# Optimization experiments

Measured on AMD Instinct MI355X. Metric: run time of the kernel, lower is better.

## Reference

```python
import jax, jax.numpy as jnp
import numpy as np

V, E, H, L, B, S = 32000, 256, 512, 2, 128, 512


def _lstm_step(x, h, c, w_ih, w_hh, b_ih, b_hh):
    # PyTorch gate order: i, f, g, o
    gates = x @ w_ih.T + b_ih + h @ w_hh.T + b_hh
    i, f, g, o = jnp.split(gates, 4, axis=-1)
    c2 = jax.nn.sigmoid(f) * c + jax.nn.sigmoid(i) * jnp.tanh(g)
    h2 = jax.nn.sigmoid(o) * jnp.tanh(c2)
    return h2, c2


def setup_inputs() -> dict:
    key = jax.random.key(0)
    ks = jax.random.split(key, 16)
    s = 0.05
    d = {}
    d["dec_input"] = jax.random.randint(ks[0], (B,), 0, V)
    d["hidden"] = jax.random.normal(ks[1], (L, B, H), jnp.float32)
    d["cell"] = jax.random.normal(ks[2], (L, B, H), jnp.float32)
    d["encoder_outputs"] = jax.random.normal(ks[3], (S, B, H), jnp.float32)
    d["emb"] = jax.random.normal(ks[4], (V, E), jnp.float32) * s
    d["attn_w"] = jax.random.normal(ks[5], (1, 2 * H), jnp.float32) * s
    d["attn_b"] = jnp.zeros((1,), jnp.float32)
    d["w_ih0"] = jax.random.normal(ks[6], (4 * H, E + H), jnp.float32) * s
    d["w_hh0"] = jax.random.normal(ks[7], (4 * H, H), jnp.float32) * s
    d["b_ih0"] = jnp.zeros((4 * H,), jnp.float32)
    d["b_hh0"] = jnp.zeros((4 * H,), jnp.float32)
    d["w_ih1"] = jax.random.normal(ks[8], (4 * H, H), jnp.float32) * s
    d["w_hh1"] = jax.random.normal(ks[9], (4 * H, H), jnp.float32) * s
    d["b_ih1"] = jnp.zeros((4 * H,), jnp.float32)
    d["b_hh1"] = jnp.zeros((4 * H,), jnp.float32)
    d["fc_w"] = jax.random.normal(ks[10], (V, H), jnp.float32) * s
    d["fc_b"] = jnp.zeros((V,), jnp.float32)
    return d


def reference(dec_input, hidden, cell, encoder_outputs, emb, attn_w, attn_b,
              w_ih0, w_hh0, b_ih0, b_hh0, w_ih1, w_hh1, b_ih1, b_hh1,
              fc_w, fc_b):
    # embedded: [B, E]  (dropout p=0 -> identity)
    embedded = emb[dec_input]
    # Bahdanau-style additive scoring using FIRST-layer hidden (as in source)
    h0 = hidden[0]                                   # [B, H]
    w_enc, w_hid = attn_w[0, :H], attn_w[0, H:]      # split linear over concat
    # logits[b,s] = enc[s,b]@w_enc + h0[b]@w_hid + b
    logits = jnp.einsum('sbh,h->bs', encoder_outputs, w_enc) \
        + (h0 @ w_hid)[:, None] + attn_b[0]          # [B, S]
    alpha = jax.nn.softmax(logits, axis=1)           # softmax over src positions
    # context = sum_s alpha[b,s] * enc[s,b,:]  (avoids repeat_interleave blowup)
    context = jnp.einsum('bs,sbh->bh', alpha, encoder_outputs)  # [B, H]
    x = jnp.concatenate([context, embedded], axis=1)            # [B, H+E]
    # single-timestep 2-layer LSTM
    h_0, c_0 = _lstm_step(x, hidden[0], cell[0], w_ih0, w_hh0, b_ih0, b_hh0)
    h_1, c_1 = _lstm_step(h_0, hidden[1], cell[1], w_ih1, w_hh1, b_ih1, b_hh1)
    new_hidden = jnp.stack([h_0, h_1])
    new_cell = jnp.stack([c_0, c_1])
    prediction = h_1 @ fc_w.T + fc_b                 # [B, V]
    return prediction, new_hidden, new_cell
```

## Files before the change

### kernel.cpp

```cpp
#include <hip/hip_runtime.h>
#include <hip/hip_bf16.h>
#include <math.h>

constexpr int NV = 32000;
constexpr int NE = 256;
constexpr int NH = 512;
constexpr int NB = 128;
constexpr int NS = 512;
constexpr int NX = NH + NE;
constexpr int NG = 2048;
constexpr int NSC = 8;

typedef __attribute__((ext_vector_type(8))) short short8;
typedef __attribute__((ext_vector_type(4))) short short4v;
typedef __attribute__((ext_vector_type(4))) float f32x4;

constexpr size_t OFF_PCTX  = 0;
constexpr size_t OFF_PML   = OFF_PCTX  + (size_t)NB*NSC*NH;
constexpr size_t OFF_XBF   = OFF_PML   + (size_t)NB*NSC*2;
constexpr size_t OFF_H0NBF = OFF_XBF   + 49152;
constexpr size_t OFF_H1NBF = OFF_H0NBF + 32768;
constexpr size_t OFF_H0BFI = OFF_H1NBF + 32768;
constexpr size_t OFF_H1BFI = OFF_H0BFI + 32768;
constexpr size_t OFF_GBUF  = OFF_H1BFI + 32768;

constexpr size_t OUT_HID  = (size_t)NB * NV;
constexpr size_t OUT_CELL = OUT_HID + 2ull * NB * NH;

__device__ inline float sigf(float x) { return 1.0f / (1.0f + expf(-x)); }
__device__ inline short bf16s(float x) {
  __hip_bfloat16 h = __float2bfloat16(x);
  return *reinterpret_cast<short*>(&h);
}

__global__ __launch_bounds__(256) void attn_partial_k(
    const float* __restrict__ enc, const float* __restrict__ attn_w,
    float* __restrict__ pctx, float* __restrict__ pml) {
  const int sc = blockIdx.x, b = blockIdx.y;
  const int wv = threadIdx.x >> 6, lane = threadIdx.x & 63;
  const f32x4 wa = *reinterpret_cast<const f32x4*>(attn_w + lane * 4);
  const f32x4 wb = *reinterpret_cast<const f32x4*>(attn_w + 256 + lane * 4);
  float m0 = -INFINITY, l0 = 0.f, m1 = -INFINITY, l1 = 0.f;
  f32x4 a00 = {}, a01 = {}, a10 = {}, a11 = {};
  const float* base = enc + ((size_t)(sc * 64 + wv) * NB + b) * NH;
  for (int i = 0; i < 8; ++i) {
    const float* r0 = base + (size_t)(i * 4) * NB * NH;
    const float* r1 = base + (size_t)((i + 8) * 4) * NB * NH;
    f32x4 e00 = *reinterpret_cast<const f32x4*>(r0 + lane * 4);
    f32x4 e01 = *reinterpret_cast<const f32x4*>(r0 + 256 + lane * 4);
    f32x4 e10 = *reinterpret_cast<const f32x4*>(r1 + lane * 4);
    f32x4 e11 = *reinterpret_cast<const f32x4*>(r1 + 256 + lane * 4);
    float d0 = e00.x * wa.x + e00.y * wa.y + e00.z * wa.z + e00.w * wa.w
             + e01.x * wb.x + e01.y * wb.y + e01.z * wb.z + e01.w * wb.w;
    float d1 = e10.x * wa.x + e10.y * wa.y + e10.z * wa.z + e10.w * wa.w
             + e11.x * wb.x + e11.y * wb.y + e11.z * wb.z + e11.w * wb.w;
#pragma unroll
    for (int off = 32; off; off >>= 1) {
      d0 += __shfl_xor(d0, off);
      d1 += __shfl_xor(d1, off);
    }
    float mn0 = fmaxf(m0, d0), mn1 = fmaxf(m1, d1);
    float s0 = expf(m0 - mn0), s1 = expf(m1 - mn1);
    float p0 = expf(d0 - mn0), p1 = expf(d1 - mn1);
    l0 = l0 * s0 + p0;         l1 = l1 * s1 + p1;
    a00 = a00 * s0 + p0 * e00; a01 = a01 * s0 + p0 * e01;
    a10 = a10 * s1 + p1 * e10; a11 = a11 * s1 + p1 * e11;
    m0 = mn0; m1 = mn1;
  }
  const float Mw = fmaxf(m0, m1);
  const float c0 = expf(m0 - Mw), c1 = expf(m1 - Mw);
  const float lw = l0 * c0 + l1 * c1;
  const f32x4 accA = a00 * c0 + a10 * c1;
  const f32x4 accB = a01 * c0 + a11 * c1;
  __shared__ float sm[4], sl[4], sacc[4][NH];
  if (lane == 0) { sm[wv] = Mw; sl[wv] = lw; }
  *reinterpret_cast<f32x4*>(&sacc[wv][lane * 4]) = accA;
  *reinterpret_cast<f32x4*>(&sacc[wv][256 + lane * 4]) = accB;
  __syncthreads();
  const float M = fmaxf(fmaxf(sm[0], sm[1]), fmaxf(sm[2], sm[3]));
  const float e0 = expf(sm[0] - M), e1 = expf(sm[1] - M),
              e2 = expf(sm[2] - M), e3 = expf(sm[3] - M);
  const int t = threadIdx.x;
  float* outc = pctx + ((size_t)b * NSC + sc) * NH;
#pragma unroll
  for (int q = 0; q < 2; ++q) {
    int h = q * 256 + t;
    outc[h] = sacc[0][h] * e0 + sacc[1][h] * e1 + sacc[2][h] * e2 + sacc[3][h] * e3;
  }
  if (t == 0) {
    pml[((size_t)b * NSC + sc) * 2 + 0] = M;
    pml[((size_t)b * NSC + sc) * 2 + 1] = sl[0] * e0 + sl[1] * e1 + sl[2] * e2 + sl[3] * e3;
  }
}

__global__ __launch_bounds__(256) void attn_finish_k(
    const float* __restrict__ pctx, const float* __restrict__ pml,
    const float* __restrict__ emb, const int* __restrict__ dec,
    const float* __restrict__ hidden,
    __hip_bfloat16* __restrict__ xbf,
    __hip_bfloat16* __restrict__ h0bf, __hip_bfloat16* __restrict__ h1bf) {
  const int b = blockIdx.x, t = threadIdx.x;
  float ms[NSC];
  float M = -INFINITY;
#pragma unroll
  for (int sc = 0; sc < NSC; ++sc) {
    ms[sc] = pml[((size_t)b * NSC + sc) * 2 + 0];
    M = fmaxf(M, ms[sc]);
  }
  float L = 0.f, es[NSC];
#pragma unroll
  for (int sc = 0; sc < NSC; ++sc) {
    es[sc] = expf(ms[sc] - M);
    L += pml[((size_t)b * NSC + sc) * 2 + 1] * es[sc];
  }
  const float invL = 1.f / L;
#pragma unroll
  for (int q = 0; q < 2; ++q) {
    int h = q * 256 + t;
    float v = 0.f;
#pragma unroll
    for (int sc = 0; sc < NSC; ++sc)
      v += pctx[((size_t)b * NSC + sc) * NH + h] * es[sc];
    xbf[(size_t)b * NX + h] = __float2bfloat16(v * invL);
    h0bf[(size_t)b * NH + h] = __float2bfloat16(hidden[(size_t)b * NH + h]);
    h1bf[(size_t)b * NH + h] =
        __float2bfloat16(hidden[(size_t)(NB * NH) + (size_t)b * NH + h]);
  }
  xbf[(size_t)b * NX + NH + t] = __float2bfloat16(emb[(size_t)dec[b] * NE + t]);
}

constexpr int LSLAB = 520;
__global__ __launch_bounds__(256, 1) void lstm_gemm_k(
    const float* __restrict__ Wx, int Kx, const float* __restrict__ Wh,
    const __hip_bfloat16* __restrict__ Ax, const __hip_bfloat16* __restrict__ Ah,
    float* __restrict__ gbuf) {
  __shared__ short wlds[2][8 * LSLAB];
  const int tid = threadIdx.x, wv = tid >> 6, lane = tid & 63;
  const int l15 = lane & 15, lhi = lane >> 4;
  const int n0 = blockIdx.x * 16;
  const int NCHX = Kx >> 8, NCH = NCHX + 2;
  const int srow = tid >> 6;
  const int scol = lane * 4;
  const int soff0 = (scol >> 5) * LSLAB + (scol & 31);

  f32x4 wr[4];
#define LSTAGE_LOAD(c)                                                        \
  {                                                                           \
    const bool fx = (c) < NCHX;                                               \
    const float* Ws = fx ? Wx : Wh;                                           \
    const int Ks = fx ? Kx : NH;                                              \
    const int cb = fx ? (c) * 256 : ((c) - NCHX) * 256;                       \
    _Pragma("unroll")                                                         \
    for (int i = 0; i < 4; ++i)                                               \
      wr[i] = *reinterpret_cast<const f32x4*>(                                \
          Ws + (size_t)(n0 + i * 4 + srow) * Ks + cb + scol);                 \
  }
#define LSTAGE_WRITE(buf)                                                     \
  {                                                                           \
    _Pragma("unroll")                                                         \
    for (int i = 0; i < 4; ++i) {                                             \
      short4v cv;                                                             \
      cv[0] = bf16s(wr[i].x); cv[1] = bf16s(wr[i].y);                         \
      cv[2] = bf16s(wr[i].z); cv[3] = bf16s(wr[i].w);                         \
      *reinterpret_cast<short4v*>((buf) + soff0 + (i * 4 + srow) * 32) = cv;  \
    }                                                                         \
  }

  LSTAGE_LOAD(0);
  LSTAGE_WRITE(wlds[0]);
  __syncthreads();

  f32x4 acc0 = {}, acc1 = {};
  for (int c = 0; c < NCH; ++c) {
    if (c + 1 < NCH) LSTAGE_LOAD(c + 1);
    {
      const bool fx = c < NCHX;
      const __hip_bfloat16* As = fx ? Ax : Ah;
      const int Ks = fx ? Kx : NH;
      const int cb = fx ? c * 256 : (c - NCHX) * 256;
      const short* wb = wlds[c & 1];
      const __hip_bfloat16* ar0 = As + (size_t)(wv * 32 + l15) * Ks + cb + lhi * 8;
      const __hip_bfloat16* ar1 = ar0 + (size_t)16 * Ks;
#pragma unroll
      for (int ks = 0; ks < 8; ++ks) {
        short8 bf = *reinterpret_cast<const short8*>(wb + ks * LSLAB + l15 * 32 + lhi * 8);
        short8 a0 = *reinterpret_cast<const short8*>(ar0 + ks * 32);
        short8 a1 = *reinterpret_cast<const short8*>(ar1 + ks * 32);
        acc0 = __builtin_amdgcn_mfma_f32_16x16x32_bf16(a0, bf, acc0, 0, 0, 0);
        acc1 = __builtin_amdgcn_mfma_f32_16x16x32_bf16(a1, bf, acc1, 0, 0, 0);
      }
    }
    if (c + 1 < NCH) {
      LSTAGE_WRITE(wlds[(c + 1) & 1]);
      __syncthreads();
    }
  }
#pragma unroll
  for (int q = 0; q < 4; ++q) {
    gbuf[(size_t)(wv * 32 + lhi * 4 + q) * NG + n0 + l15] = acc0[q];
    gbuf[(size_t)(wv * 32 + 16 + lhi * 4 + q) * NG + n0 + l15] = acc1[q];
  }
#undef LSTAGE_LOAD
#undef LSTAGE_WRITE
}

__global__ __launch_bounds__(256) void lstm_point_k(
    const float* __restrict__ g, const float* __restrict__ b_ih,
    const float* __restrict__ b_hh, const float* __restrict__ c_in,
    float* __restrict__ h_out, float* __restrict__ c_out,
    __hip_bfloat16* __restrict__ hbf_out) {
  const int idx = blockIdx.x * 256 + threadIdx.x;
  const int h = idx & 511;
  const size_t base = (size_t)(idx >> 9) * NG;
  float ig = g[base + 0 * NH + h] + b_ih[0 * NH + h] + b_hh[0 * NH + h];
  float fg = g[base + 1 * NH + h] + b_ih[1 * NH + h] + b_hh[1 * NH + h];
  float gg = g[base + 2 * NH + h] + b_ih[2 * NH + h] + b_hh[2 * NH + h];
  float og = g[base + 3 * NH + h] + b_ih[3 * NH + h] + b_hh[3 * NH + h];
  float c = c_in[idx];
  float c2 = sigf(fg) * c + sigf(ig) * tanhf(gg);
  float h2 = sigf(og) * tanhf(c2);
  c_out[idx] = c2;
  h_out[idx] = h2;
  hbf_out[idx] = __float2bfloat16(h2);
}

constexpr int FC_PANELS = 8;
constexpr int FC_BLOCKS = NV / (16 * FC_PANELS);
constexpr int SLAB = 520;

__global__ __launch_bounds__(256, 1) void gemm_fc_pipe_k(
    const __hip_bfloat16* __restrict__ Abf, const float* __restrict__ W,
    const float* __restrict__ bias, float* __restrict__ out) {
  __shared__ short wlds[2][16 * SLAB];
  const int tid = threadIdx.x, wv = tid >> 6, lane = tid & 63;
  const int l15 = lane & 15, lhi = lane >> 4;
  const int nbase = blockIdx.x * (16 * FC_PANELS);

  int soff[8];
#pragma unroll
  for (int i = 0; i < 8; ++i) {
    const int o = i * 1024 + tid * 4;
    const int n = o >> 9, kk = o & 511;
    soff[i] = (kk >> 5) * SLAB + n * 32 + (kk & 31);
  }

  short8 af[2][16];
#pragma unroll
  for (int m = 0; m < 2; ++m) {
    const __hip_bfloat16* ar = Abf + (size_t)(wv * 32 + m * 16 + l15) * NH + lhi * 8;
#pragma unroll
    for (int ks = 0; ks < 16; ++ks)
      af[m][ks] = *reinterpret_cast<const short8*>(ar + ks * 32);
  }

  f32x4 wr[8];
  {
    const float* panel = W + (size_t)nbase * NH;
#pragma unroll
    for (int i = 0; i < 8; ++i)
      wr[i] = *reinterpret_cast<const f32x4*>(panel + i * 1024 + tid * 4);
    short* wb0 = wlds[0];
#pragma unroll
    for (int i = 0; i < 8; ++i) {
      short4v cv;
      cv[0] = bf16s(wr[i].x); cv[1] = bf16s(wr[i].y);
      cv[2] = bf16s(wr[i].z); cv[3] = bf16s(wr[i].w);
      *reinterpret_cast<short4v*>(wb0 + soff[i]) = cv;
    }
  }
  __syncthreads();

  f32x4 s0 = {}, s1 = {};
  int sn0 = -1;
  for (int p = 0; p < FC_PANELS; ++p) {
    if (p < FC_PANELS - 1) {
      const float* panel = W + (size_t)(nbase + (p + 1) * 16) * NH;
#pragma unroll
      for (int i = 0; i < 8; ++i)
        wr[i] = *reinterpret_cast<const f32x4*>(panel + i * 1024 + tid * 4);
    }
    if (sn0 >= 0) {
      const float bv = bias[sn0 + l15];
#pragma unroll
      for (int q = 0; q < 4; ++q) {
        out[(size_t)(wv * 32 + 0 * 16 + lhi * 4 + q) * NV + sn0 + l15] = s0[q] + bv;
        out[(size_t)(wv * 32 + 1 * 16 + lhi * 4 + q) * NV + sn0 + l15] = s1[q] + bv;
      }
    }
    {
      const short* wb = wlds[p & 1];
      f32x4 a0 = {}, a1 = {};
#pragma unroll
      for (int ks = 0; ks < 16; ++ks) {
        short8 bf = *reinterpret_cast<const short8*>(wb + ks * SLAB + l15 * 32 + lhi * 8);
        a0 = __builtin_amdgcn_mfma_f32_16x16x32_bf16(af[0][ks], bf, a0, 0, 0, 0);
        a1 = __builtin_amdgcn_mfma_f32_16x16x32_bf16(af[1][ks], bf, a1, 0, 0, 0);
      }
      s0 = a0; s1 = a1; sn0 = nbase + p * 16;
    }
    if (p < FC_PANELS - 1) {
      short* wbn = wlds[(p + 1) & 1];
#pragma unroll
      for (int i = 0; i < 8; ++i) {
        short4v cv;
        cv[0] = bf16s(wr[i].x); cv[1] = bf16s(wr[i].y);
        cv[2] = bf16s(wr[i].z); cv[3] = bf16s(wr[i].w);
        *reinterpret_cast<short4v*>(wbn + soff[i]) = cv;
      }
      __syncthreads();
    }
  }
  {
    const float bv = bias[sn0 + l15];
#pragma unroll
    for (int q = 0; q < 4; ++q) {
      out[(size_t)(wv * 32 + 0 * 16 + lhi * 4 + q) * NV + sn0 + l15] = s0[q] + bv;
      out[(size_t)(wv * 32 + 1 * 16 + lhi * 4 + q) * NV + sn0 + l15] = s1[q] + bv;
    }
  }
}

extern "C" void kernel_launch(void* const* d_in, const int* in_sizes, int n_in,
                              void* d_out, int out_size, void* d_ws, size_t ws_size,
                              hipStream_t stream) {
  const int*   dec    = (const int*)d_in[0];
  const float* hidden = (const float*)d_in[1];
  const float* cell   = (const float*)d_in[2];
  const float* enc    = (const float*)d_in[3];
  const float* emb    = (const float*)d_in[4];
  const float* attn_w = (const float*)d_in[5];
  const float* w_ih0  = (const float*)d_in[7];
  const float* w_hh0  = (const float*)d_in[8];
  const float* b_ih0  = (const float*)d_in[9];
  const float* b_hh0  = (const float*)d_in[10];
  const float* w_ih1  = (const float*)d_in[11];
  const float* w_hh1  = (const float*)d_in[12];
  const float* b_ih1  = (const float*)d_in[13];
  const float* b_hh1  = (const float*)d_in[14];
  const float* fc_w   = (const float*)d_in[15];
  const float* fc_b   = (const float*)d_in[16];
  float* out = (float*)d_out;
  float* ws  = (float*)d_ws;

  float* pctx = ws + OFF_PCTX;
  float* pml  = ws + OFF_PML;
  __hip_bfloat16* xbf   = (__hip_bfloat16*)(ws + OFF_XBF);
  __hip_bfloat16* h0nbf = (__hip_bfloat16*)(ws + OFF_H0NBF);
  __hip_bfloat16* h1nbf = (__hip_bfloat16*)(ws + OFF_H1NBF);
  __hip_bfloat16* h0bf  = (__hip_bfloat16*)(ws + OFF_H0BFI);
  __hip_bfloat16* h1bf  = (__hip_bfloat16*)(ws + OFF_H1BFI);
  float* gbuf = ws + OFF_GBUF;

  attn_partial_k<<<dim3(NSC, NB), 256, 0, stream>>>(enc, attn_w, pctx, pml);
  attn_finish_k<<<NB, 256, 0, stream>>>(pctx, pml, emb, dec, hidden,
                                        xbf, h0bf, h1bf);
  lstm_gemm_k<<<NG / 16, 256, 0, stream>>>(w_ih0, NX, w_hh0, xbf, h0bf, gbuf);
  lstm_point_k<<<NB * NH / 256, 256, 0, stream>>>(gbuf, b_ih0, b_hh0, cell,
                                                  out + OUT_HID, out + OUT_CELL,
                                                  h0nbf);
  lstm_gemm_k<<<NG / 16, 256, 0, stream>>>(w_ih1, NH, w_hh1, h0nbf, h1bf, gbuf);
  lstm_point_k<<<NB * NH / 256, 256, 0, stream>>>(gbuf, b_ih1, b_hh1,
                                                  cell + NB * NH,
                                                  out + OUT_HID + (size_t)NB * NH,
                                                  out + OUT_CELL + (size_t)NB * NH,
                                                  h1nbf);
  gemm_fc_pipe_k<<<FC_BLOCKS, 256, 0, stream>>>(h1nbf, fc_w, fc_b, out);
}
```

Baseline: 78.53 us.

## Fuse LSTM gate GEMM with pointwise cell update via gate-interleaved column tiles

Each LSTM GEMM block now computes 4 hidden units across all four gates (rows i*NH + p*4 + srow), so it holds complete gate sets. It stages results in shared memory and applies the cell/hidden update in-kernel. This removes the gbuf round trip through global memory and two kernel launches. The block count and weight tile shape stay the same (128 blocks of 16 columns), with an extra barrier and pointwise work added at the tail.

```diff
diff --git a/kernel.cpp b/kernel.cpp
--- a/kernel.cpp
+++ b/kernel.cpp
@@ -8,7 +8,6 @@
 constexpr int NB = 128;
 constexpr int NS = 512;
 constexpr int NX = NH + NE;
-constexpr int NG = 2048;
 constexpr int NSC = 8;
 
 typedef __attribute__((ext_vector_type(8))) short short8;
@@ -22,7 +21,6 @@
 constexpr size_t OFF_H1NBF = OFF_H0NBF + 32768;
 constexpr size_t OFF_H0BFI = OFF_H1NBF + 32768;
 constexpr size_t OFF_H1BFI = OFF_H0BFI + 32768;
-constexpr size_t OFF_GBUF  = OFF_H1BFI + 32768;
 
 constexpr size_t OUT_HID  = (size_t)NB * NV;
 constexpr size_t OUT_CELL = OUT_HID + 2ull * NB * NH;
@@ -130,14 +128,18 @@
 }
 
 constexpr int LSLAB = 520;
-__global__ __launch_bounds__(256, 1) void lstm_gemm_k(
+__global__ __launch_bounds__(256, 1) void lstm_fused_k(
     const float* __restrict__ Wx, int Kx, const float* __restrict__ Wh,
     const __hip_bfloat16* __restrict__ Ax, const __hip_bfloat16* __restrict__ Ah,
-    float* __restrict__ gbuf) {
+    const float* __restrict__ b_ih, const float* __restrict__ b_hh,
+    const float* __restrict__ c_in,
+    float* __restrict__ h_out, float* __restrict__ c_out,
+    __hip_bfloat16* __restrict__ hbf_out) {
   __shared__ short wlds[2][8 * LSLAB];
+  __shared__ float sg[NB][17];
   const int tid = threadIdx.x, wv = tid >> 6, lane = tid & 63;
   const int l15 = lane & 15, lhi = lane >> 4;
-  const int n0 = blockIdx.x * 16;
+  const int p = blockIdx.x;
   const int NCHX = Kx >> 8, NCH = NCHX + 2;
   const int srow = tid >> 6;
   const int scol = lane * 4;
@@ -153,7 +155,7 @@
     _Pragma("unroll")                                                         \
     for (int i = 0; i < 4; ++i)                                               \
       wr[i] = *reinterpret_cast<const f32x4*>(                                \
-          Ws + (size_t)(n0 + i * 4 + srow) * Ks + cb + scol);                 \
+          Ws + (size_t)(i * NH + p * 4 + srow) * Ks + cb + scol);             \
   }
 #define LSTAGE_WRITE(buf)                                                     \
   {                                                                           \
@@ -197,31 +199,28 @@
   }
 #pragma unroll
   for (int q = 0; q < 4; ++q) {
-    gbuf[(size_t)(wv * 32 + lhi * 4 + q) * NG + n0 + l15] = acc0[q];
-    gbuf[(size_t)(wv * 32 + 16 + lhi * 4 + q) * NG + n0 + l15] = acc1[q];
+    sg[wv * 32 + lhi * 4 + q][l15] = acc0[q];
+    sg[wv * 32 + 16 + lhi * 4 + q][l15] = acc1[q];
+  }
+  __syncthreads();
+#pragma unroll
+  for (int it = 0; it < 2; ++it) {
+    const int item = tid + it * 256;
+    const int b = item >> 2, r = item & 3;
+    const int h = p * 4 + r;
+    float ig = sg[b][0 + r]  + b_ih[0 * NH + h] + b_hh[0 * NH + h];
+    float fg = sg[b][4 + r]  + b_ih[1 * NH + h] + b_hh[1 * NH + h];
+    float gg = sg[b][8 + r]  + b_ih[2 * NH + h] + b_hh[2 * NH + h];
+    float og = sg[b][12 + r] + b_ih[3 * NH + h] + b_hh[3 * NH + h];
+    float c = c_in[(size_t)b * NH + h];
+    float c2 = sigf(fg) * c + sigf(ig) * tanhf(gg);
+    float h2 = sigf(og) * tanhf(c2);
+    c_out[(size_t)b * NH + h] = c2;
+    h_out[(size_t)b * NH + h] = h2;
+    hbf_out[(size_t)b * NH + h] = __float2bfloat16(h2);
   }
 #undef LSTAGE_LOAD
 #undef LSTAGE_WRITE
-}
-
-__global__ __launch_bounds__(256) void lstm_point_k(
-    const float* __restrict__ g, const float* __restrict__ b_ih,
-    const float* __restrict__ b_hh, const float* __restrict__ c_in,
-    float* __restrict__ h_out, float* __restrict__ c_out,
-    __hip_bfloat16* __restrict__ hbf_out) {
-  const int idx = blockIdx.x * 256 + threadIdx.x;
-  const int h = idx & 511;
-  const size_t base = (size_t)(idx >> 9) * NG;
-  float ig = g[base + 0 * NH + h] + b_ih[0 * NH + h] + b_hh[0 * NH + h];
-  float fg = g[base + 1 * NH + h] + b_ih[1 * NH + h] + b_hh[1 * NH + h];
-  float gg = g[base + 2 * NH + h] + b_ih[2 * NH + h] + b_hh[2 * NH + h];
-  float og = g[base + 3 * NH + h] + b_ih[3 * NH + h] + b_hh[3 * NH + h];
-  float c = c_in[idx];
-  float c2 = sigf(fg) * c + sigf(ig) * tanhf(gg);
-  float h2 = sigf(og) * tanhf(c2);
-  c_out[idx] = c2;
-  h_out[idx] = h2;
-  hbf_out[idx] = __float2bfloat16(h2);
 }
 
 constexpr int FC_PANELS = 8;
@@ -349,20 +348,16 @@
   __hip_bfloat16* h1nbf = (__hip_bfloat16*)(ws + OFF_H1NBF);
   __hip_bfloat16* h0bf  = (__hip_bfloat16*)(ws + OFF_H0BFI);
   __hip_bfloat16* h1bf  = (__hip_bfloat16*)(ws + OFF_H1BFI);
-  float* gbuf = ws + OFF_GBUF;
 
   attn_partial_k<<<dim3(NSC, NB), 256, 0, stream>>>(enc, attn_w, pctx, pml);
   attn_finish_k<<<NB, 256, 0, stream>>>(pctx, pml, emb, dec, hidden,
                                         xbf, h0bf, h1bf);
-  lstm_gemm_k<<<NG / 16, 256, 0, stream>>>(w_ih0, NX, w_hh0, xbf, h0bf, gbuf);
-  lstm_point_k<<<NB * NH / 256, 256, 0, stream>>>(gbuf, b_ih0, b_hh0, cell,
-                                                  out + OUT_HID, out + OUT_CELL,
-                                                  h0nbf);
-  lstm_gemm_k<<<NG / 16, 256, 0, stream>>>(w_ih1, NH, w_hh1, h0nbf, h1bf, gbuf);
-  lstm_point_k<<<NB * NH / 256, 256, 0, stream>>>(gbuf, b_ih1, b_hh1,
-                                                  cell + NB * NH,
-                                                  out + OUT_HID + (size_t)NB * NH,
-                                                  out + OUT_CELL + (size_t)NB * NH,
-                                                  h1nbf);
+  lstm_fused_k<<<NH / 4, 256, 0, stream>>>(w_ih0, NX, w_hh0, xbf, h0bf,
+                                           b_ih0, b_hh0, cell,
+                                           out + OUT_HID, out + OUT_CELL, h0nbf);
+  lstm_fused_k<<<NH / 4, 256, 0, stream>>>(w_ih1, NH, w_hh1, h0nbf, h1bf,
+                                           b_ih1, b_hh1, cell + NB * NH,
+                                           out + OUT_HID + (size_t)NB * NH,
+                                           out + OUT_CELL + (size_t)NB * NH, h1nbf);
   gemm_fc_pipe_k<<<FC_BLOCKS, 256, 0, stream>>>(h1nbf, fc_w, fc_b, out);
 }
```

Measured after the change: 76.76 us. 1.02x faster.
